# Optimization experiments

Hardware: AMD Instinct MI355X
Metric: run time of the kernel (lower is better)

## Reference

```python
import jax, jax.numpy as jnp
import numpy as np

B, S, L = 32, 16, 64            # batch, sentences/doc, words/sentence
V, E, P, H = 32000, 300, 100, 256  # vocab, embed_dim, position_dim, hidden_dim
D_ATT = 2 * H + P               # 612, word/sentence attention dim
POL = 3


def _lstm(x, Wih, Whh, b):
    # x: [N, T, Din]; Wih: [4H, Din]; Whh: [4H, H]; b: [4H]
    N = x.shape[0]
    Hh = Whh.shape[1]
    g_pre = jnp.einsum('ntd,gd->ntg', x, Wih) + b  # precompute input gates

    def step(carry, g):
        h, c = carry
        gates = g + h @ Whh.T
        i, f, gg, o = jnp.split(gates, 4, axis=-1)
        c = jax.nn.sigmoid(f) * c + jax.nn.sigmoid(i) * jnp.tanh(gg)
        h = jax.nn.sigmoid(o) * jnp.tanh(c)
        return (h, c), h

    init = (jnp.zeros((N, Hh), x.dtype), jnp.zeros((N, Hh), x.dtype))
    (hT, _), hs = jax.lax.scan(step, init, jnp.swapaxes(g_pre, 0, 1))
    return jnp.swapaxes(hs, 0, 1), hT  # [N,T,H], [N,H]


def _bilstm(x, Wih_f, Whh_f, b_f, Wih_b, Whh_b, b_b):
    out_f, h_f = _lstm(x, Wih_f, Whh_f, b_f)
    out_b, h_b = _lstm(x[:, ::-1], Wih_b, Whh_b, b_b)
    return jnp.concatenate([out_f, out_b[:, ::-1]], -1), h_f, h_b


def _attn_pool(h, pos, W, b, proj):
    # h: [N,T,2H], pos: [N,T,P]; tanh([h;pos] @ W + b) @ proj -> softmax over T
    z = jnp.concatenate([h, pos], -1)
    u = jnp.tanh(jnp.einsum('ntd,de->nte', z, W) + b)
    a = jax.nn.softmax(jnp.einsum('ntd,d->nt', u, proj), axis=-1)
    return jnp.einsum('nt,nth->nh', a, h)


def setup_inputs() -> dict:
    key = jax.random.key(0)
    ks = jax.random.split(key, 32)
    sc = 0.05

    def rn(k, shape):
        return jax.random.normal(k, shape, dtype=jnp.float32) * sc

    inp = {
        'text_raw_indices': jax.random.randint(ks[0], (B, S, L), 1, V),
        'word_position': jax.random.randint(ks[1], (B, S, L), 0, 1005),
        'segment_position': jax.random.randint(ks[2], (B, S), 0, 25),
        'emb': rn(ks[3], (V, E)),
        'wpos_emb': rn(ks[4], (1005, P)),
        'spos_emb': rn(ks[5], (25, P)),
        # word-level BiLSTM (input = E + P = 400)
        'wWih_f': rn(ks[6], (4 * H, E + P)), 'wWhh_f': rn(ks[7], (4 * H, H)), 'wb_f': rn(ks[8], (4 * H,)),
        'wWih_b': rn(ks[9], (4 * H, E + P)), 'wWhh_b': rn(ks[10], (4 * H, H)), 'wb_b': rn(ks[11], (4 * H,)),
        # sentence-level BiLSTM (input = 2H + P = 612)
        'sWih_f': rn(ks[12], (4 * H, D_ATT)), 'sWhh_f': rn(ks[13], (4 * H, H)), 'sb_f': rn(ks[14], (4 * H,)),
        'sWih_b': rn(ks[15], (4 * H, D_ATT)), 'sWhh_b': rn(ks[16], (4 * H, H)), 'sb_b': rn(ks[17], (4 * H,)),
        # word attention
        'word_W': rn(ks[18], (D_ATT, D_ATT)), 'word_bias': rn(ks[19], (D_ATT,)), 'word_proj': rn(ks[20], (D_ATT,)),
        # sentence attention
        'sent_W': rn(ks[21], (D_ATT, D_ATT)), 'sent_bias': rn(ks[22], (D_ATT,)), 'sent_proj': rn(ks[23], (D_ATT,)),
        # classifier
        'dense_W': rn(ks[24], (POL, 4 * H)), 'dense_b': rn(ks[25], (POL,)),
    }
    return inp


def reference(text_raw_indices, word_position, segment_position,
              emb, wpos_emb, spos_emb,
              wWih_f, wWhh_f, wb_f, wWih_b, wWhh_b, wb_b,
              sWih_f, sWhh_f, sb_f, sWih_b, sWhh_b, sb_b,
              word_W, word_bias, word_proj,
              sent_W, sent_bias, sent_proj,
              dense_W, dense_b):
    bs = text_raw_indices.shape[0]
    tokens = text_raw_indices.reshape(-1, L)          # [B*S, L]
    wpos = word_position.reshape(-1, L)               # [B*S, L]

    wpe = wpos_emb[wpos]                              # [B*S, L, P]
    x = jnp.concatenate([emb[tokens], wpe], -1)       # [B*S, L, E+P]

    sen_out, _, _ = _bilstm(x, wWih_f, wWhh_f, wb_f, wWih_b, wWhh_b, wb_b)  # [B*S,L,2H]
    sen_vec = _attn_pool(sen_out, wpe, word_W, word_bias, word_proj)        # [B*S,2H]

    spe = spos_emb[segment_position]                  # [B, S, P]
    sx = jnp.concatenate([sen_vec.reshape(bs, S, 2 * H), spe], -1)          # [B,S,2H+P]

    doc_out, dh_f, dh_b = _bilstm(sx, sWih_f, sWhh_f, sb_f, sWih_b, sWhh_b, sb_b)
    doc_vec = _attn_pool(doc_out, spe, sent_W, sent_bias, sent_proj)        # [B,2H]

    last_doc = jnp.concatenate([dh_f, dh_b], -1)      # [B,2H]
    feats = jnp.concatenate([doc_vec, last_doc], -1)  # [B,4H]
    return feats @ dense_W.T + dense_b                # [B,POL]
```

## Files before the change

kernel.cpp:

```cpp
#include <hip/hip_runtime.h>
#include <hip/hip_bf16.h>

#define B_    32
#define S_    16
#define L_    64
#define E_    300
#define P_    100
#define H_    256
#define DATT  612
#define NS    512
#define M1    32768

typedef __hip_bfloat16 hbf;
typedef __attribute__((ext_vector_type(8))) short bf16x8;
typedef __attribute__((ext_vector_type(4))) float f32x4;
typedef __attribute__((ext_vector_type(4))) int i32x4;

__device__ __forceinline__ float u2f(unsigned short u) {
    unsigned int x = ((unsigned int)u) << 16;
    return __builtin_bit_cast(float, x);
}
__device__ __forceinline__ unsigned short f2u(float f) {
    return __builtin_bit_cast(unsigned short, __float2bfloat16(f));
}
__device__ __forceinline__ float sigm(float x) { return 1.0f / (1.0f + __expf(-x)); }
__device__ __forceinline__ float tanh_f(float x) {
    return 1.0f - 2.0f / (__expf(2.0f * x) + 1.0f);
}

__global__ void k_prep_wih(const float* __restrict__ wf, const float* __restrict__ wb,
                           int Ksrc, int Kdst, unsigned short* __restrict__ out) {
    int j = blockIdx.x;
    const float* src = (j < 1024) ? (wf + (size_t)j * Ksrc) : (wb + (size_t)(j - 1024) * Ksrc);
    unsigned short* o = out + (size_t)j * Kdst;
    for (int c = threadIdx.x; c < Kdst; c += blockDim.x)
        o[c] = (c < Ksrc) ? f2u(src[c]) : (unsigned short)0;
}

__global__ void k_cat_bias(const float* __restrict__ a, const float* __restrict__ b,
                           float* __restrict__ dst) {
    int i = blockIdx.x * 256 + threadIdx.x;
    dst[i] = (i < 1024) ? a[i] : b[i - 1024];
}

__global__ void k_prep_whhr(const float* __restrict__ w0, const float* __restrict__ w1,
                            const float* __restrict__ w2, const float* __restrict__ w3,
                            unsigned short* __restrict__ out) {
    const float* w;
    switch (blockIdx.y) { case 0: w = w0; break; case 1: w = w1; break;
                          case 2: w = w2; break; default: w = w3; }
    int fi = blockIdx.x;
    int wv = fi >> 6, cf = (fi >> 3) & 7, kt = fi & 7;
    int lane = threadIdx.x;
    int l16 = lane & 15, kqq = lane >> 4;
    int col = (cf & 3) * 256 + wv * 32 + (cf >> 2) * 16 + l16;
    int kbase = kt * 32 + kqq * 8;
    size_t obase = ((size_t)blockIdx.y * 512 + fi) * 512 + (size_t)lane * 8;
    #pragma unroll
    for (int e = 0; e < 8; ++e)
        out[obase + e] = f2u(w[(size_t)col * 256 + kbase + e]);
}

__global__ void k_prep_attw(const float* __restrict__ W, unsigned short* __restrict__ out) {
    int n = blockIdx.x;
    for (int k = threadIdx.x; k < 640; k += blockDim.x)
        out[(size_t)n * 640 + k] = (n < DATT && k < DATT) ? f2u(W[(size_t)k * DATT + n]) : (unsigned short)0;
}

__global__ void k_gather_x(const int* __restrict__ tok, const int* __restrict__ wpos,
                           const float* __restrict__ emb, const float* __restrict__ wpe,
                           unsigned short* __restrict__ x) {
    int i = blockIdx.x;
    int t = tok[i], p = wpos[i];
    const float* er = emb + (size_t)t * E_;
    const float* pr = wpe + (size_t)p * P_;
    unsigned short* xr = x + (size_t)i * 416;
    for (int c = threadIdx.x; c < 416; c += blockDim.x) {
        float v = (c < E_) ? er[c] : (c < 400 ? pr[c - E_] : 0.f);
        xr[c] = f2u(v);
    }
}

__global__ __launch_bounds__(256) void k_gemm_bias(
        const unsigned short* __restrict__ A, int lda,
        const unsigned short* __restrict__ W, const float* __restrict__ bias,
        unsigned short* __restrict__ C, int nkt) {
    __shared__ __align__(16) unsigned short As[128][40];
    __shared__ __align__(16) unsigned short Bs[128][40];
    int tid = threadIdx.x;
    int lane = tid & 63, wave = tid >> 6;
    int wm = wave >> 1, wn = wave & 1;
    int i0 = blockIdx.y * 128, n0 = blockIdx.x * 128;
    f32x4 acc[4][4] = {};
    int r = tid >> 2, kc = (tid & 3) * 8;
    for (int kt = 0; kt < nkt; ++kt) {
        int k0 = kt * 32;
        #pragma unroll
        for (int p = 0; p < 2; ++p) {
            int rr = r + p * 64;
            *(i32x4*)&As[rr][kc] = *(const i32x4*)&A[(size_t)(i0 + rr) * lda + k0 + kc];
            *(i32x4*)&Bs[rr][kc] = *(const i32x4*)&W[(size_t)(n0 + rr) * lda + k0 + kc];
        }
        __syncthreads();
        bf16x8 a[4], b[4];
        int arow = wm * 64 + (lane & 15);
        int brow = wn * 64 + (lane & 15);
        int kq = (lane >> 4) * 8;
        #pragma unroll
        for (int mi = 0; mi < 4; ++mi) a[mi] = *(const bf16x8*)&As[arow + mi * 16][kq];
        #pragma unroll
        for (int nj = 0; nj < 4; ++nj) b[nj] = *(const bf16x8*)&Bs[brow + nj * 16][kq];
        #pragma unroll
        for (int mi = 0; mi < 4; ++mi)
            #pragma unroll
            for (int nj = 0; nj < 4; ++nj)
                acc[mi][nj] = __builtin_amdgcn_mfma_f32_16x16x32_bf16(a[mi], b[nj], acc[mi][nj], 0, 0, 0);
        __syncthreads();
    }
    int q = lane >> 4;
    #pragma unroll
    for (int nj = 0; nj < 4; ++nj) {
        int col = n0 + wn * 64 + nj * 16 + (lane & 15);
        float bb = bias[col];
        #pragma unroll
        for (int mi = 0; mi < 4; ++mi)
            #pragma unroll
            for (int rr2 = 0; rr2 < 4; ++rr2) {
                int grow = i0 + wm * 64 + mi * 16 + q * 4 + rr2;
                C[(size_t)grow * 2048 + col] = f2u(acc[mi][nj][rr2] + bb);
            }
    }
}

__global__ __launch_bounds__(256) void k_attn_mfma(
        const unsigned short* __restrict__ Hsrc,
        const unsigned short* __restrict__ xpos,
        const float* __restrict__ spe, const int* __restrict__ spos,
        const unsigned short* __restrict__ Wt,
        const float* __restrict__ bias, const float* __restrict__ proj,
        float* __restrict__ score, int mode) {
    __shared__ __align__(16) unsigned short As[128][40];
    __shared__ __align__(16) unsigned short Bs[128][40];
    int tid = threadIdx.x;
    int lane = tid & 63, wave = tid >> 6;
    int wm = wave >> 1, wn = wave & 1;
    int i0 = blockIdx.y * 128, n0 = blockIdx.x * 128;
    f32x4 acc[4][4] = {};
    int r = tid >> 2, kc = (tid & 3) * 8;
    for (int kt = 0; kt < 20; ++kt) {
        int k0 = kt * 32;
        #pragma unroll
        for (int p = 0; p < 2; ++p) {
            int rr = r + p * 64;
            if (kt < 16) {
                *(i32x4*)&As[rr][kc] = *(const i32x4*)&Hsrc[(size_t)(i0 + rr) * 512 + k0 + kc];
            } else {
                int grow = i0 + rr;
                #pragma unroll
                for (int e = 0; e < 8; ++e) {
                    int k = k0 + kc + e;
                    int pp = k - 512;
                    unsigned short v = 0;
                    if (pp < P_) {
                        if (mode == 0) v = xpos[(size_t)grow * 416 + 300 + pp];
                        else           v = f2u(spe[(size_t)spos[grow] * P_ + pp]);
                    }
                    As[rr][kc + e] = v;
                }
            }
            *(i32x4*)&Bs[rr][kc] = *(const i32x4*)&Wt[(size_t)(n0 + rr) * 640 + k0 + kc];
        }
        __syncthreads();
        bf16x8 a[4], b[4];
        int arow = wm * 64 + (lane & 15);
        int brow = wn * 64 + (lane & 15);
        int kq = (lane >> 4) * 8;
        #pragma unroll
        for (int mi = 0; mi < 4; ++mi) a[mi] = *(const bf16x8*)&As[arow + mi * 16][kq];
        #pragma unroll
        for (int nj = 0; nj < 4; ++nj) b[nj] = *(const bf16x8*)&Bs[brow + nj * 16][kq];
        #pragma unroll
        for (int mi = 0; mi < 4; ++mi)
            #pragma unroll
            for (int nj = 0; nj < 4; ++nj)
                acc[mi][nj] = __builtin_amdgcn_mfma_f32_16x16x32_bf16(a[mi], b[nj], acc[mi][nj], 0, 0, 0);
        __syncthreads();
    }
    float srow[4][4] = {};
    int q = lane >> 4;
    #pragma unroll
    for (int nj = 0; nj < 4; ++nj) {
        int col = n0 + wn * 64 + nj * 16 + (lane & 15);
        if (col < DATT) {
            float bb = bias[col], pp = proj[col];
            #pragma unroll
            for (int mi = 0; mi < 4; ++mi)
                #pragma unroll
                for (int rr2 = 0; rr2 < 4; ++rr2)
                    srow[mi][rr2] += pp * tanh_f(acc[mi][nj][rr2] + bb);
        }
    }
    #pragma unroll
    for (int mi = 0; mi < 4; ++mi)
        #pragma unroll
        for (int rr2 = 0; rr2 < 4; ++rr2) {
            float v = srow[mi][rr2];
            v += __shfl_xor(v, 1); v += __shfl_xor(v, 2);
            v += __shfl_xor(v, 4); v += __shfl_xor(v, 8);
            if ((lane & 15) == 0)
                atomicAdd(&score[i0 + wm * 64 + mi * 16 + q * 4 + rr2], v);
        }
}

__global__ __launch_bounds__(512, 2) void k_lstm_res(
        const unsigned short* __restrict__ g,
        const unsigned short* __restrict__ whhr,
        unsigned short* __restrict__ out,
        float* __restrict__ finalh,
        int T) {
    extern __shared__ __align__(16) char smem[];
    char* wlds = smem;
    unsigned short* gpre = (unsigned short*)(smem + 147456);
    unsigned short* hbuf = (unsigned short*)(smem + 155648);
    const int tid = threadIdx.x;
    const int lane = tid & 63, w = tid >> 6;
    const int l16 = lane & 15, kq = lane >> 4;
    const int dir = blockIdx.y;
    const int seq0 = blockIdx.x * 4;
    const unsigned short* wsrc = whhr + (size_t)dir * (512 * 512);

    for (int i = tid; i < 5 * 264; i += 512) hbuf[i] = 0;

    bf16x8 wreg[46];
    char* wlds_w = wlds + w * 18432;
    #pragma unroll
    for (int cf = 0; cf < 8; ++cf) {
        #pragma unroll
        for (int kt = 0; kt < 8; ++kt) {
            const int FI = cf * 8 + kt;
            const unsigned short* src = wsrc + ((size_t)(w * 8 + cf) * 8 + kt) * 512 + (size_t)lane * 8;
            if (FI < 46) wreg[FI] = *(const bf16x8*)src;
            else *(i32x4*)(wlds_w + (FI - 46) * 1024 + lane * 16) = *(const i32x4*)src;
        }
    }
    float c[2][4] = {};
    const int gseq = tid >> 7, gcol = (tid & 127) * 8;
    i32x4 gld = *(const i32x4*)&g[((size_t)(seq0 + gseq) * T + (dir ? (T - 1) : 0)) * 2048
                                  + dir * 1024 + gcol];
    __syncthreads();

    const char* hrow = (const char*)hbuf + (l16 < 4 ? l16 : 4) * 528 + kq * 16;
    for (int t = 0; t < T; ++t) {
        const int ti = dir ? (T - 1 - t) : t;
        f32x4 acc[8] = {};
        #pragma unroll
        for (int kt = 0; kt < 8; ++kt) {
            bf16x8 a = *(const bf16x8*)(hrow + kt * 64);
            #pragma unroll
            for (int cf = 0; cf < 8; ++cf) {
                const int FI = cf * 8 + kt;
                bf16x8 b;
                if (FI < 46) b = wreg[FI];
                else b = *(const bf16x8*)(wlds_w + (FI - 46) * 1024 + lane * 16);
                acc[cf] = __builtin_amdgcn_mfma_f32_16x16x32_bf16(a, b, acc[cf], 0, 0, 0);
            }
        }
        *(i32x4*)&gpre[gseq * 1024 + gcol] = gld;
        __syncthreads();
        if (kq == 0) {
            bool last = (t == T - 1);
            #pragma unroll
            for (int u16 = 0; u16 < 2; ++u16) {
                const int u = w * 32 + u16 * 16 + l16;
                #pragma unroll
                for (int rr = 0; rr < 4; ++rr) {
                    float ig = acc[u16 * 4 + 0][rr] + u2f(gpre[rr * 1024 + u]);
                    float fg = acc[u16 * 4 + 1][rr] + u2f(gpre[rr * 1024 + 256 + u]);
                    float gg = acc[u16 * 4 + 2][rr] + u2f(gpre[rr * 1024 + 512 + u]);
                    float og = acc[u16 * 4 + 3][rr] + u2f(gpre[rr * 1024 + 768 + u]);
                    ig = sigm(ig); fg = sigm(fg); gg = tanh_f(gg); og = sigm(og);
                    c[u16][rr] = fg * c[u16][rr] + ig * gg;
                    float hn = og * tanh_f(c[u16][rr]);
                    unsigned short hnb = f2u(hn);
                    hbuf[rr * 264 + u] = hnb;
                    out[((size_t)(seq0 + rr) * T + ti) * 512 + dir * 256 + u] = hnb;
                    if (finalh && last)
                        finalh[(size_t)(seq0 + rr) * 1024 + dir * 256 + u] = hn;
                }
            }
        }
        __syncthreads();
        if (t + 1 < T) {
            const int tn = dir ? (T - 2 - t) : (t + 1);
            gld = *(const i32x4*)&g[((size_t)(seq0 + gseq) * T + tn) * 2048 + dir * 1024 + gcol];
        }
    }
}

__global__ void k_pool_word(const float* __restrict__ score, const unsigned short* __restrict__ sen_out,
                            const float* __restrict__ spe, const int* __restrict__ spos,
                            unsigned short* __restrict__ sx) {
    int n = blockIdx.x, tid = threadIdx.x;
    __shared__ float a_lds[64];
    if (tid < 64) {
        float sc = score[n * 64 + tid];
        float m = sc;
        #pragma unroll
        for (int off = 32; off >= 1; off >>= 1) m = fmaxf(m, __shfl_xor(m, off));
        float e = __expf(sc - m);
        float s = e;
        #pragma unroll
        for (int off = 32; off >= 1; off >>= 1) s += __shfl_xor(s, off);
        a_lds[tid] = e / s;
    }
    __syncthreads();
    for (int h = tid; h < 512; h += blockDim.x) {
        float acc = 0.f;
        const unsigned short* base = sen_out + (size_t)n * 64 * 512 + h;
        #pragma unroll 8
        for (int t = 0; t < 64; ++t) acc += a_lds[t] * u2f(base[(size_t)t * 512]);
        sx[(size_t)n * 640 + h] = f2u(acc);
    }
    int sp = spos[n];
    for (int p2 = tid; p2 < 128; p2 += blockDim.x)
        sx[(size_t)n * 640 + 512 + p2] = (p2 < P_) ? f2u(spe[(size_t)sp * P_ + p2]) : (unsigned short)0;
}

__global__ void k_pool_sent(const float* __restrict__ score, const unsigned short* __restrict__ doc_out,
                            float* __restrict__ feats) {
    int n = blockIdx.x, tid = threadIdx.x;
    __shared__ float a_lds[16];
    if (tid < 16) {
        float sc = score[n * 16 + tid];
        float m = sc;
        #pragma unroll
        for (int off = 8; off >= 1; off >>= 1) m = fmaxf(m, __shfl_xor(m, off));
        float e = __expf(sc - m);
        float s = e;
        #pragma unroll
        for (int off = 8; off >= 1; off >>= 1) s += __shfl_xor(s, off);
        a_lds[tid] = e / s;
    }
    __syncthreads();
    for (int h = tid; h < 512; h += blockDim.x) {
        float acc = 0.f;
        const unsigned short* base = doc_out + (size_t)n * 16 * 512 + h;
        #pragma unroll
        for (int t = 0; t < 16; ++t) acc += a_lds[t] * u2f(base[(size_t)t * 512]);
        feats[(size_t)n * 1024 + h] = acc;
    }
}

__global__ void k_dense(const float* __restrict__ feats, const float* __restrict__ W,
                        const float* __restrict__ bias, float* __restrict__ out) {
    int b = blockIdx.x, lane = threadIdx.x;
    for (int p = 0; p < 3; ++p) {
        float acc = 0.f;
        for (int k = lane; k < 1024; k += 64)
            acc += feats[(size_t)b * 1024 + k] * W[(size_t)p * 1024 + k];
        #pragma unroll
        for (int off = 32; off >= 1; off >>= 1) acc += __shfl_xor(acc, off);
        if (lane == 0) out[b * 3 + p] = acc + bias[p];
    }
}

extern "C" void kernel_launch(void* const* d_in, const int* in_sizes, int n_in,
                              void* d_out, int out_size, void* d_ws, size_t ws_size,
                              hipStream_t stream) {
    const int*   tok    = (const int*)d_in[0];
    const int*   wpos   = (const int*)d_in[1];
    const int*   spos   = (const int*)d_in[2];
    const float* emb    = (const float*)d_in[3];
    const float* wpet   = (const float*)d_in[4];
    const float* spet   = (const float*)d_in[5];
    const float* wWih_f = (const float*)d_in[6];
    const float* wWhh_f = (const float*)d_in[7];
    const float* wb_f   = (const float*)d_in[8];
    const float* wWih_b = (const float*)d_in[9];
    const float* wWhh_b = (const float*)d_in[10];
    const float* wb_b   = (const float*)d_in[11];
    const float* sWih_f = (const float*)d_in[12];
    const float* sWhh_f = (const float*)d_in[13];
    const float* sb_f   = (const float*)d_in[14];
    const float* sWih_b = (const float*)d_in[15];
    const float* sWhh_b = (const float*)d_in[16];
    const float* sb_b   = (const float*)d_in[17];
    const float* word_W = (const float*)d_in[18];
    const float* word_bias = (const float*)d_in[19];
    const float* word_proj = (const float*)d_in[20];
    const float* sent_W = (const float*)d_in[21];
    const float* sent_bias = (const float*)d_in[22];
    const float* sent_proj = (const float*)d_in[23];
    const float* dense_W = (const float*)d_in[24];
    const float* dense_b = (const float*)d_in[25];

    char* p = (char*)d_ws;
    auto alloc = [&](size_t bytes) -> void* {
        void* r = (void*)p;
        p += (bytes + 255) & ~(size_t)255;
        return r;
    };
    unsigned short* x_bf    = (unsigned short*)alloc((size_t)M1 * 416 * 2);
    unsigned short* g_bf    = (unsigned short*)alloc((size_t)M1 * 2048 * 2);
    unsigned short* sen_out = (unsigned short*)alloc((size_t)M1 * 512 * 2);
    float*          scores  = (float*)alloc((size_t)(M1 + NS) * 4);
    unsigned short* sx      = (unsigned short*)alloc((size_t)NS * 640 * 2);
    unsigned short* sg      = (unsigned short*)alloc((size_t)NS * 2048 * 2);
    unsigned short* doc_out = (unsigned short*)alloc((size_t)NS * 512 * 2);
    float*          feats   = (float*)alloc((size_t)B_ * 1024 * 4);
    unsigned short* wih_w   = (unsigned short*)alloc((size_t)2048 * 416 * 2);
    unsigned short* wih_s   = (unsigned short*)alloc((size_t)2048 * 640 * 2);
    float*          bias_w  = (float*)alloc(2048 * 4);
    float*          bias_s  = (float*)alloc(2048 * 4);
    unsigned short* whh_r   = (unsigned short*)alloc((size_t)4 * 512 * 512 * 2);
    unsigned short* attw_w  = (unsigned short*)alloc((size_t)640 * 640 * 2);
    unsigned short* attw_s  = (unsigned short*)alloc((size_t)640 * 640 * 2);
    float* wscore = scores;
    float* sscore = scores + M1;

    hipMemsetAsync(scores, 0, (size_t)(M1 + NS) * 4, stream);
    k_prep_wih<<<2048, 256, 0, stream>>>(wWih_f, wWih_b, 400, 416, wih_w);
    k_prep_wih<<<2048, 256, 0, stream>>>(sWih_f, sWih_b, 612, 640, wih_s);
    k_cat_bias<<<8, 256, 0, stream>>>(wb_f, wb_b, bias_w);
    k_cat_bias<<<8, 256, 0, stream>>>(sb_f, sb_b, bias_s);
    k_prep_whhr<<<dim3(512, 4), 64, 0, stream>>>(wWhh_f, wWhh_b, sWhh_f, sWhh_b, whh_r);
    k_prep_attw<<<640, 256, 0, stream>>>(word_W, attw_w);
    k_prep_attw<<<640, 256, 0, stream>>>(sent_W, attw_s);
    k_gather_x<<<M1, 256, 0, stream>>>(tok, wpos, emb, wpet, x_bf);

    const unsigned int lstm_lds = 147456 + 8192 + 5 * 264 * 2;

    k_gemm_bias<<<dim3(16, 256), 256, 0, stream>>>(x_bf, 416, wih_w, bias_w, g_bf, 13);
    k_lstm_res<<<dim3(128, 2), 512, lstm_lds, stream>>>(g_bf, whh_r, sen_out, nullptr, L_);
    k_attn_mfma<<<dim3(5, 256), 256, 0, stream>>>(sen_out, x_bf, nullptr, nullptr,
                                                  attw_w, word_bias, word_proj, wscore, 0);
    k_pool_word<<<512, 256, 0, stream>>>(wscore, sen_out, spet, spos, sx);

    k_gemm_bias<<<dim3(16, 4), 256, 0, stream>>>(sx, 640, wih_s, bias_s, sg, 20);
    k_lstm_res<<<dim3(8, 2), 512, lstm_lds, stream>>>(sg, whh_r + (size_t)2 * 512 * 512,
                                                      doc_out, feats + 512, S_);
    k_attn_mfma<<<dim3(5, 4), 256, 0, stream>>>(doc_out, nullptr, spet, spos,
                                                attw_s, sent_bias, sent_proj, sscore, 1);
    k_pool_sent<<<32, 256, 0, stream>>>(sscore, doc_out, feats);

    k_dense<<<32, 64, 0, stream>>>(feats, dense_W, dense_b, (float*)d_out);
}
```

Before: 884.9 us.

## Restructure LSTM recurrence to 4 waves holding more Whh in registers

The recurrent LSTM kernel moves from 8 waves of 512 threads to 4 waves of 256 threads. Each wave now owns 64 hidden units and keeps 96 of its 128 weight fragments in registers, with the rest in LDS, so fewer weight bytes are read from LDS each step. Gate pre-activations are staged through an LDS buffer so every thread handles one hidden unit across all four sequences in the elementwise update. This trades very high register pressure and half as many threads for the MFMA chain against less LDS weight traffic. The final hidden state is now written once after the loop from the bf16 h buffer, so finalh takes bf16-rounded values instead of fp32.

```diff
diff --git a/kernel.cpp b/kernel.cpp
--- a/kernel.cpp
+++ b/kernel.cpp
@@ -50,10 +50,10 @@
     switch (blockIdx.y) { case 0: w = w0; break; case 1: w = w1; break;
                           case 2: w = w2; break; default: w = w3; }
     int fi = blockIdx.x;
-    int wv = fi >> 6, cf = (fi >> 3) & 7, kt = fi & 7;
+    int wv = fi >> 7, cf = (fi >> 3) & 15, kt = fi & 7;
     int lane = threadIdx.x;
     int l16 = lane & 15, kqq = lane >> 4;
-    int col = (cf & 3) * 256 + wv * 32 + (cf >> 2) * 16 + l16;
+    int col = (cf & 3) * 256 + wv * 64 + (cf >> 2) * 16 + l16;
     int kbase = kt * 32 + kqq * 8;
     size_t obase = ((size_t)blockIdx.y * 512 + fi) * 512 + (size_t)lane * 8;
     #pragma unroll
@@ -212,7 +212,7 @@
         }
 }
 
-__global__ __launch_bounds__(512, 2) void k_lstm_res(
+__global__ __launch_bounds__(256, 1) void k_lstm_res(
         const unsigned short* __restrict__ g,
         const unsigned short* __restrict__ whhr,
         unsigned short* __restrict__ out,
@@ -220,6 +220,7 @@
         int T) {
     extern __shared__ __align__(16) char smem[];
     char* wlds = smem;
+    float* gates = (float*)(smem + 131072);
     unsigned short* gpre = (unsigned short*)(smem + 147456);
     unsigned short* hbuf = (unsigned short*)(smem + 155648);
     const int tid = threadIdx.x;
@@ -229,71 +230,104 @@
     const int seq0 = blockIdx.x * 4;
     const unsigned short* wsrc = whhr + (size_t)dir * (512 * 512);
 
-    for (int i = tid; i < 5 * 264; i += 512) hbuf[i] = 0;
-
-    bf16x8 wreg[46];
-    char* wlds_w = wlds + w * 18432;
-    #pragma unroll
-    for (int cf = 0; cf < 8; ++cf) {
+    for (int i = tid; i < 5 * 264; i += 256) hbuf[i] = 0;
+
+    bf16x8 wreg[96];
+    char* wlds_w = wlds + w * 32768;
+    #pragma unroll
+    for (int cf = 0; cf < 16; ++cf) {
         #pragma unroll
         for (int kt = 0; kt < 8; ++kt) {
-            const int FI = cf * 8 + kt;
-            const unsigned short* src = wsrc + ((size_t)(w * 8 + cf) * 8 + kt) * 512 + (size_t)lane * 8;
-            if (FI < 46) wreg[FI] = *(const bf16x8*)src;
-            else *(i32x4*)(wlds_w + (FI - 46) * 1024 + lane * 16) = *(const i32x4*)src;
-        }
-    }
-    float c[2][4] = {};
-    const int gseq = tid >> 7, gcol = (tid & 127) * 8;
-    i32x4 gld = *(const i32x4*)&g[((size_t)(seq0 + gseq) * T + (dir ? (T - 1) : 0)) * 2048
-                                  + dir * 1024 + gcol];
+            const int fi = cf * 8 + kt;
+            const unsigned short* src = wsrc + (((size_t)(w * 16 + cf) * 8 + kt) << 9) + (size_t)lane * 8;
+            if (fi < 96) wreg[fi] = *(const bf16x8*)src;
+            else *(i32x4*)(wlds_w + (fi - 96) * 1024 + lane * 16) = *(const i32x4*)src;
+        }
+    }
+    float c[4] = {0.f, 0.f, 0.f, 0.f};
+
+    i32x4 gld[2];
+    #pragma unroll
+    for (int it = 0; it < 2; ++it) {
+        int idx = tid + it * 256;
+        int sq = idx >> 7, ch = idx & 127;
+        gld[it] = *(const i32x4*)&g[((size_t)(seq0 + sq) * T + (dir ? T - 1 : 0)) * 2048
+                                    + dir * 1024 + ch * 8];
+    }
     __syncthreads();
 
     const char* hrow = (const char*)hbuf + (l16 < 4 ? l16 : 4) * 528 + kq * 16;
     for (int t = 0; t < T; ++t) {
         const int ti = dir ? (T - 1 - t) : t;
-        f32x4 acc[8] = {};
-        #pragma unroll
-        for (int kt = 0; kt < 8; ++kt) {
-            bf16x8 a = *(const bf16x8*)(hrow + kt * 64);
-            #pragma unroll
-            for (int cf = 0; cf < 8; ++cf) {
-                const int FI = cf * 8 + kt;
-                bf16x8 b;
-                if (FI < 46) b = wreg[FI];
-                else b = *(const bf16x8*)(wlds_w + (FI - 46) * 1024 + lane * 16);
-                acc[cf] = __builtin_amdgcn_mfma_f32_16x16x32_bf16(a, b, acc[cf], 0, 0, 0);
-            }
-        }
-        *(i32x4*)&gpre[gseq * 1024 + gcol] = gld;
-        __syncthreads();
-        if (kq == 0) {
-            bool last = (t == T - 1);
-            #pragma unroll
-            for (int u16 = 0; u16 < 2; ++u16) {
-                const int u = w * 32 + u16 * 16 + l16;
-                #pragma unroll
-                for (int rr = 0; rr < 4; ++rr) {
-                    float ig = acc[u16 * 4 + 0][rr] + u2f(gpre[rr * 1024 + u]);
-                    float fg = acc[u16 * 4 + 1][rr] + u2f(gpre[rr * 1024 + 256 + u]);
-                    float gg = acc[u16 * 4 + 2][rr] + u2f(gpre[rr * 1024 + 512 + u]);
-                    float og = acc[u16 * 4 + 3][rr] + u2f(gpre[rr * 1024 + 768 + u]);
-                    ig = sigm(ig); fg = sigm(fg); gg = tanh_f(gg); og = sigm(og);
-                    c[u16][rr] = fg * c[u16][rr] + ig * gg;
-                    float hn = og * tanh_f(c[u16][rr]);
-                    unsigned short hnb = f2u(hn);
-                    hbuf[rr * 264 + u] = hnb;
-                    out[((size_t)(seq0 + rr) * T + ti) * 512 + dir * 256 + u] = hnb;
-                    if (finalh && last)
-                        finalh[(size_t)(seq0 + rr) * 1024 + dir * 256 + u] = hn;
-                }
-            }
-        }
-        __syncthreads();
+        #pragma unroll
+        for (int it = 0; it < 2; ++it) {
+            int idx = tid + it * 256;
+            int sq = idx >> 7, ch = idx & 127;
+            *(i32x4*)&gpre[sq * 1024 + ch * 8] = gld[it];
+        }
         if (t + 1 < T) {
             const int tn = dir ? (T - 2 - t) : (t + 1);
-            gld = *(const i32x4*)&g[((size_t)(seq0 + gseq) * T + tn) * 2048 + dir * 1024 + gcol];
-        }
+            #pragma unroll
+            for (int it = 0; it < 2; ++it) {
+                int idx = tid + it * 256;
+                int sq = idx >> 7, ch = idx & 127;
+                gld[it] = *(const i32x4*)&g[((size_t)(seq0 + sq) * T + tn) * 2048
+                                            + dir * 1024 + ch * 8];
+            }
+        }
+        #pragma unroll
+        for (int half = 0; half < 2; ++half) {
+            f32x4 acc[8] = {};
+            #pragma unroll
+            for (int kt = 0; kt < 8; ++kt) {
+                bf16x8 a = *(const bf16x8*)(hrow + kt * 64);
+                #pragma unroll
+                for (int cc = 0; cc < 8; ++cc) {
+                    const int cf = half * 8 + cc;
+                    const int fi = cf * 8 + kt;
+                    bf16x8 b;
+                    if (fi < 96) b = wreg[fi];
+                    else b = *(const bf16x8*)(wlds_w + (fi - 96) * 1024 + lane * 16);
+                    acc[cc] = __builtin_amdgcn_mfma_f32_16x16x32_bf16(a, b, acc[cc], 0, 0, 0);
+                }
+            }
+            if (kq == 0) {
+                #pragma unroll
+                for (int cc = 0; cc < 8; ++cc) {
+                    const int cf = half * 8 + cc;
+                    int col = (cf & 3) * 256 + w * 64 + (cf >> 2) * 16 + l16;
+                    *(f32x4*)&gates[col * 4] = acc[cc];
+                }
+            }
+        }
+        __syncthreads();
+        {
+            const int u = tid;
+            f32x4 gi = *(const f32x4*)&gates[(0 * 256 + u) * 4];
+            f32x4 gf = *(const f32x4*)&gates[(1 * 256 + u) * 4];
+            f32x4 gc = *(const f32x4*)&gates[(2 * 256 + u) * 4];
+            f32x4 go = *(const f32x4*)&gates[(3 * 256 + u) * 4];
+            #pragma unroll
+            for (int s = 0; s < 4; ++s) {
+                float ig = gi[s] + u2f(gpre[s * 1024 + u]);
+                float fg = gf[s] + u2f(gpre[s * 1024 + 256 + u]);
+                float gv = gc[s] + u2f(gpre[s * 1024 + 512 + u]);
+                float og = go[s] + u2f(gpre[s * 1024 + 768 + u]);
+                ig = sigm(ig); fg = sigm(fg); gv = tanh_f(gv); og = sigm(og);
+                c[s] = fg * c[s] + ig * gv;
+                float hn = og * tanh_f(c[s]);
+                unsigned short hnb = f2u(hn);
+                hbuf[s * 264 + u] = hnb;
+                out[((size_t)(seq0 + s) * T + ti) * 512 + dir * 256 + u] = hnb;
+            }
+        }
+        __syncthreads();
+    }
+    if (finalh) {
+        const int u = tid;
+        #pragma unroll
+        for (int s = 0; s < 4; ++s)
+            finalh[(size_t)(seq0 + s) * 1024 + dir * 256 + u] = u2f(hbuf[s * 264 + u]);
     }
 }
 
@@ -428,16 +462,16 @@
     k_prep_attw<<<640, 256, 0, stream>>>(sent_W, attw_s);
     k_gather_x<<<M1, 256, 0, stream>>>(tok, wpos, emb, wpet, x_bf);
 
-    const unsigned int lstm_lds = 147456 + 8192 + 5 * 264 * 2;
+    const unsigned int lstm_lds = 131072 + 16384 + 8192 + 5 * 264 * 2;
 
     k_gemm_bias<<<dim3(16, 256), 256, 0, stream>>>(x_bf, 416, wih_w, bias_w, g_bf, 13);
-    k_lstm_res<<<dim3(128, 2), 512, lstm_lds, stream>>>(g_bf, whh_r, sen_out, nullptr, L_);
+    k_lstm_res<<<dim3(128, 2), 256, lstm_lds, stream>>>(g_bf, whh_r, sen_out, nullptr, L_);
     k_attn_mfma<<<dim3(5, 256), 256, 0, stream>>>(sen_out, x_bf, nullptr, nullptr,
                                                   attw_w, word_bias, word_proj, wscore, 0);
     k_pool_word<<<512, 256, 0, stream>>>(wscore, sen_out, spet, spos, sx);
 
     k_gemm_bias<<<dim3(16, 4), 256, 0, stream>>>(sx, 640, wih_s, bias_s, sg, 20);
-    k_lstm_res<<<dim3(8, 2), 512, lstm_lds, stream>>>(sg, whh_r + (size_t)2 * 512 * 512,
+    k_lstm_res<<<dim3(8, 2), 256, lstm_lds, stream>>>(sg, whh_r + (size_t)2 * 512 * 512,
                                                       doc_out, feats + 512, S_);
     k_attn_mfma<<<dim3(5, 4), 256, 0, stream>>>(doc_out, nullptr, spet, spos,
                                                 attw_s, sent_bias, sent_proj, sscore, 1);
```

Result: faster. 736.9 us (-16.7%).

## Batch 16 sequences per LSTM block and keep all Whh fragments in registers

Applied to the files above, without the earlier changes.

The recurrent LSTM kernel now processes 16 sequences per block instead of 4, so all 16 rows of each MFMA tile carry real work and all four lane groups take part in the gate math. The full recurrent weight slice is held in registers, using inline asm so that most fragments sit in AGPRs, which removes the LDS weight cache. The pre-gate prefetch is moved before the MFMAs, and the final hidden state is written once after the loop. This leaves 4x fewer blocks (64 for the word-level LSTM, 4 for the sentence-level one), lowering parallelism, and it carries heavy register pressure.

```diff
diff --git a/kernel.cpp b/kernel.cpp
--- a/kernel.cpp
+++ b/kernel.cpp
@@ -219,80 +219,92 @@
         float* __restrict__ finalh,
         int T) {
     extern __shared__ __align__(16) char smem[];
-    char* wlds = smem;
-    unsigned short* gpre = (unsigned short*)(smem + 147456);
-    unsigned short* hbuf = (unsigned short*)(smem + 155648);
+    unsigned short* gpre = (unsigned short*)smem;
+    unsigned short* hbuf = (unsigned short*)(smem + 32768);
     const int tid = threadIdx.x;
     const int lane = tid & 63, w = tid >> 6;
     const int l16 = lane & 15, kq = lane >> 4;
     const int dir = blockIdx.y;
-    const int seq0 = blockIdx.x * 4;
+    const int seq0 = blockIdx.x * 16;
     const unsigned short* wsrc = whhr + (size_t)dir * (512 * 512);
 
-    for (int i = tid; i < 5 * 264; i += 512) hbuf[i] = 0;
-
-    bf16x8 wreg[46];
-    char* wlds_w = wlds + w * 18432;
-    #pragma unroll
-    for (int cf = 0; cf < 8; ++cf) {
+    for (int i = tid; i < 16 * 272; i += 512) hbuf[i] = 0;
+
+    bf16x8 wr[64];
+    #pragma unroll
+    for (int cf = 0; cf < 8; ++cf)
         #pragma unroll
         for (int kt = 0; kt < 8; ++kt) {
-            const int FI = cf * 8 + kt;
-            const unsigned short* src = wsrc + ((size_t)(w * 8 + cf) * 8 + kt) * 512 + (size_t)lane * 8;
-            if (FI < 46) wreg[FI] = *(const bf16x8*)src;
-            else *(i32x4*)(wlds_w + (FI - 46) * 1024 + lane * 16) = *(const i32x4*)src;
-        }
-    }
+            const int fi = cf * 8 + kt;
+            wr[fi] = *(const bf16x8*)(wsrc + (((size_t)(w * 8 + cf) * 8 + kt) << 9)
+                                      + (size_t)lane * 8);
+        }
+
     float c[2][4] = {};
-    const int gseq = tid >> 7, gcol = (tid & 127) * 8;
-    i32x4 gld = *(const i32x4*)&g[((size_t)(seq0 + gseq) * T + (dir ? (T - 1) : 0)) * 2048
-                                  + dir * 1024 + gcol];
+    const int sq = tid >> 5, chb = (tid & 31) * 32;
+    i32x4 gld[4];
+    #pragma unroll
+    for (int it = 0; it < 4; ++it)
+        gld[it] = *(const i32x4*)&g[((size_t)(seq0 + sq) * T + (dir ? T - 1 : 0)) * 2048
+                                    + dir * 1024 + chb + it * 8];
     __syncthreads();
 
-    const char* hrow = (const char*)hbuf + (l16 < 4 ? l16 : 4) * 528 + kq * 16;
+    const unsigned short* hrow = hbuf + l16 * 272 + kq * 8;
     for (int t = 0; t < T; ++t) {
         const int ti = dir ? (T - 1 - t) : t;
+        #pragma unroll
+        for (int it = 0; it < 4; ++it)
+            *(i32x4*)&gpre[sq * 1024 + chb + it * 8] = gld[it];
+        if (t + 1 < T) {
+            const int tn = dir ? (T - 2 - t) : (t + 1);
+            #pragma unroll
+            for (int it = 0; it < 4; ++it)
+                gld[it] = *(const i32x4*)&g[((size_t)(seq0 + sq) * T + tn) * 2048
+                                            + dir * 1024 + chb + it * 8];
+        }
         f32x4 acc[8] = {};
         #pragma unroll
         for (int kt = 0; kt < 8; ++kt) {
-            bf16x8 a = *(const bf16x8*)(hrow + kt * 64);
+            bf16x8 a = *(const bf16x8*)(hrow + kt * 32);
             #pragma unroll
             for (int cf = 0; cf < 8; ++cf) {
-                const int FI = cf * 8 + kt;
-                bf16x8 b;
-                if (FI < 46) b = wreg[FI];
-                else b = *(const bf16x8*)(wlds_w + (FI - 46) * 1024 + lane * 16);
-                acc[cf] = __builtin_amdgcn_mfma_f32_16x16x32_bf16(a, b, acc[cf], 0, 0, 0);
+                const int fi = cf * 8 + kt;
+                if (fi < 56)
+                    asm("v_mfma_f32_16x16x32_bf16 %0, %1, %2, %0"
+                        : "+v"(acc[cf]) : "v"(a), "a"(wr[fi]));
+                else
+                    asm("v_mfma_f32_16x16x32_bf16 %0, %1, %2, %0"
+                        : "+v"(acc[cf]) : "v"(a), "v"(wr[fi]));
             }
         }
-        *(i32x4*)&gpre[gseq * 1024 + gcol] = gld;
-        __syncthreads();
-        if (kq == 0) {
-            bool last = (t == T - 1);
+        __syncthreads();
+        {
+            const int ub = w * 32 + l16;
             #pragma unroll
             for (int u16 = 0; u16 < 2; ++u16) {
-                const int u = w * 32 + u16 * 16 + l16;
+                const int u = ub + u16 * 16;
                 #pragma unroll
                 for (int rr = 0; rr < 4; ++rr) {
-                    float ig = acc[u16 * 4 + 0][rr] + u2f(gpre[rr * 1024 + u]);
-                    float fg = acc[u16 * 4 + 1][rr] + u2f(gpre[rr * 1024 + 256 + u]);
-                    float gg = acc[u16 * 4 + 2][rr] + u2f(gpre[rr * 1024 + 512 + u]);
-                    float og = acc[u16 * 4 + 3][rr] + u2f(gpre[rr * 1024 + 768 + u]);
-                    ig = sigm(ig); fg = sigm(fg); gg = tanh_f(gg); og = sigm(og);
-                    c[u16][rr] = fg * c[u16][rr] + ig * gg;
+                    const int s = kq * 4 + rr;
+                    float ig = acc[u16 * 4 + 0][rr] + u2f(gpre[s * 1024 + u]);
+                    float fg = acc[u16 * 4 + 1][rr] + u2f(gpre[s * 1024 + 256 + u]);
+                    float gv = acc[u16 * 4 + 2][rr] + u2f(gpre[s * 1024 + 512 + u]);
+                    float og = acc[u16 * 4 + 3][rr] + u2f(gpre[s * 1024 + 768 + u]);
+                    ig = sigm(ig); fg = sigm(fg); gv = tanh_f(gv); og = sigm(og);
+                    c[u16][rr] = fg * c[u16][rr] + ig * gv;
                     float hn = og * tanh_f(c[u16][rr]);
                     unsigned short hnb = f2u(hn);
-                    hbuf[rr * 264 + u] = hnb;
-                    out[((size_t)(seq0 + rr) * T + ti) * 512 + dir * 256 + u] = hnb;
-                    if (finalh && last)
-                        finalh[(size_t)(seq0 + rr) * 1024 + dir * 256 + u] = hn;
+                    hbuf[s * 272 + u] = hnb;
+                    out[((size_t)(seq0 + s) * T + ti) * 512 + dir * 256 + u] = hnb;
                 }
             }
         }
         __syncthreads();
-        if (t + 1 < T) {
-            const int tn = dir ? (T - 2 - t) : (t + 1);
-            gld = *(const i32x4*)&g[((size_t)(seq0 + gseq) * T + tn) * 2048 + dir * 1024 + gcol];
+    }
+    if (finalh) {
+        for (int i = tid; i < 16 * 256; i += 512) {
+            int s = i >> 8, u = i & 255;
+            finalh[(size_t)(seq0 + s) * 1024 + dir * 256 + u] = u2f(hbuf[s * 272 + u]);
         }
     }
 }
@@ -428,16 +440,16 @@
     k_prep_attw<<<640, 256, 0, stream>>>(sent_W, attw_s);
     k_gather_x<<<M1, 256, 0, stream>>>(tok, wpos, emb, wpet, x_bf);
 
-    const unsigned int lstm_lds = 147456 + 8192 + 5 * 264 * 2;
+    const unsigned int lstm_lds = 32768 + 16 * 272 * 2;
 
     k_gemm_bias<<<dim3(16, 256), 256, 0, stream>>>(x_bf, 416, wih_w, bias_w, g_bf, 13);
-    k_lstm_res<<<dim3(128, 2), 512, lstm_lds, stream>>>(g_bf, whh_r, sen_out, nullptr, L_);
+    k_lstm_res<<<dim3(32, 2), 512, lstm_lds, stream>>>(g_bf, whh_r, sen_out, nullptr, L_);
     k_attn_mfma<<<dim3(5, 256), 256, 0, stream>>>(sen_out, x_bf, nullptr, nullptr,
                                                   attw_w, word_bias, word_proj, wscore, 0);
     k_pool_word<<<512, 256, 0, stream>>>(wscore, sen_out, spet, spos, sx);
 
     k_gemm_bias<<<dim3(16, 4), 256, 0, stream>>>(sx, 640, wih_s, bias_s, sg, 20);
-    k_lstm_res<<<dim3(8, 2), 512, lstm_lds, stream>>>(sg, whh_r + (size_t)2 * 512 * 512,
+    k_lstm_res<<<dim3(2, 2), 512, lstm_lds, stream>>>(sg, whh_r + (size_t)2 * 512 * 512,
                                                       doc_out, feats + 512, S_);
     k_attn_mfma<<<dim3(5, 4), 256, 0, stream>>>(doc_out, nullptr, spet, spos,
                                                 attw_s, sent_bias, sent_proj, sscore, 1);
```

New measurement: 1.194 ms. 35.0% more time.
